# Optimization experiments

Hardware: AMD Instinct MI355X
Metric: run time of the kernel (lower is better)

Reference implementation:

```python
import jax, jax.numpy as jnp
import numpy as np

B, T, M, DK, DV, S = 64, 256, 64, 128, 256, 128
NSK, NQ = 200, 2000


def _glorot(k, shape):
    lim = np.sqrt(6.0 / (shape[0] + shape[1])).astype(np.float32)
    return jax.random.uniform(k, shape, jnp.float32, -lim, lim)


def setup_inputs() -> dict:
    key = jax.random.key(0)
    ks = jax.random.split(key, 16)
    tn = lambda k, shape: 0.1 * jax.random.truncated_normal(k, -2.0, 2.0, shape, jnp.float32)
    return {
        "q_data": jax.random.randint(ks[0], (B, T), 0, NSK + 1),
        "qa_data": jax.random.randint(ks[1], (B, T), 0, 2 * NSK + 1),
        "s_data": jax.random.randint(ks[2], (B, T), 0, NQ + 1),
        "key_memory": tn(ks[3], (M, DK)),
        "value_memory": tn(ks[4], (M, DV)),
        "Eq": 0.05 * jax.random.normal(ks[5], (NSK + 1, DK), jnp.float32),
        "Eqa": 0.05 * jax.random.normal(ks[6], (2 * NSK + 1, DV), jnp.float32),
        "Es": 0.05 * jax.random.normal(ks[7], (NQ + 1, DK), jnp.float32),
        "We": _glorot(ks[8], (DV, DV)), "be": jnp.zeros((DV,), jnp.float32),
        "Wa": _glorot(ks[9], (DV, DV)), "ba": jnp.zeros((DV,), jnp.float32),
        "Wsa": _glorot(ks[10], (DV, M)), "bsa": jnp.zeros((M,), jnp.float32),
        "Wqd1": _glorot(ks[11], (DK, S)), "bqd1": jnp.zeros((S,), jnp.float32),
        "Wqd": _glorot(ks[12], (S, 1)), "bqd": jnp.zeros((1,), jnp.float32),
        "Wsd1": _glorot(ks[13], (DK, S)), "bsd1": jnp.zeros((S,), jnp.float32),
        "Wsd": _glorot(ks[14], (S, 1)), "bsd": jnp.zeros((1,), jnp.float32),
    }


def reference(q_data, qa_data, s_data, key_memory, value_memory, Eq, Eqa, Es,
              We, be, Wa, ba, Wsa, bsa, Wqd1, bqd1, Wqd, bqd, Wsd1, bsd1, Wsd, bsd):
    b = q_data.shape[0]
    qe = Eq[q_data]    # [B,T,DK]
    qae = Eqa[qa_data]  # [B,T,DV]
    se = Es[s_data]    # [B,T,DK]
    # time-independent precomputation (same math, hoisted out of the loop)
    corr = jax.nn.softmax(jnp.einsum("btk,mk->btm", qe, key_memory), axis=-1)  # [B,T,M]
    erase = qae @ We + be  # [B,T,DV] (activation=None in source)
    add = qae @ Wa + ba    # [B,T,DV]
    qd = jnp.tanh(qe @ Wqd1 + bqd1) @ Wqd + bqd  # [B,T,1]
    sd = jnp.tanh(se @ Wsd1 + bsd1) @ Wsd + bsd  # [B,T,1]

    def step(Mv, x):
        cw, er, ad = x  # [B,M], [B,DV], [B,DV]
        read = jnp.einsum("bm,bmd->bd", cw, Mv)        # read BEFORE write
        sa1 = read @ Wsa + bsa                          # [B,M]
        sa = jnp.sum(cw * sa1, axis=1)                  # [B]
        scale = cw[:, :, None]                          # [B,M,1]
        Mv_new = Mv * (1.0 - er[:, None, :] * scale) + ad[:, None, :] * scale
        return Mv_new, sa

    Mv0 = jnp.broadcast_to(value_memory[None], (b,) + value_memory.shape)
    xs = (corr.transpose(1, 0, 2), erase.transpose(1, 0, 2), add.transpose(1, 0, 2))
    _, sa_t = jax.lax.scan(step, Mv0, xs)  # sa_t: [T,B]
    z = 3.0 * sa_t.T - qd[..., 0] - sd[..., 0]  # [B,T]
    return jax.nn.sigmoid(z)
```

## Files before the change

kernel.cpp:

```cpp
#include <hip/hip_runtime.h>
#include <math.h>

#define B_   64
#define T_   256
#define M_   64
#define DK_  128
#define DV_  256
#define S_   128
#define NQR  201
#define NQAR 401
#define NSR  2001

static __device__ __forceinline__ int imin(int a, int b){ return a < b ? a : b; }

static __device__ __forceinline__ float fast_tanh(float x){
  float e = __expf(2.f * x);
  return 1.f - 2.f / (e + 1.f);
}

template<int CTRL, int RM>
static __device__ __forceinline__ float dppadd(float x) {
  return x + __int_as_float(
      __builtin_amdgcn_update_dpp(0, __float_as_int(x), CTRL, RM, 0xf, true));
}
static __device__ __forceinline__ float wave_sum_lane63(float x) {
  x = dppadd<0x111, 0xf>(x);
  x = dppadd<0x112, 0xf>(x);
  x = dppadd<0x114, 0xf>(x);
  x = dppadd<0x118, 0xf>(x);
  x = dppadd<0x142, 0xa>(x);
  x = dppadd<0x143, 0xc>(x);
  return x;
}

__device__ void corr_role(int blk, const float* __restrict__ Eq,
                          const float* __restrict__ Km,
                          const float* __restrict__ Wsa,
                          const float* __restrict__ bsa,
                          float* __restrict__ corr,
                          float* __restrict__ w2_t,
                          float* __restrict__ csb_t)
{
  __shared__ float eq[4][DK_];
  __shared__ float cwb[4][M_];
  const int w = threadIdx.x >> 6, m = threadIdx.x & 63;
  const int i  = blk * 4 + w;
  const int ic = imin(i, NQR - 1);
  eq[w][m]      = Eq[ic * DK_ + m];
  eq[w][m + 64] = Eq[ic * DK_ + 64 + m];
  float acc = 0.f;
  const float4* kr = (const float4*)(Km + m * DK_);
  #pragma unroll 8
  for (int k4 = 0; k4 < DK_ / 4; ++k4) {
    float4 kv = kr[k4];
    acc = fmaf(eq[w][k4 * 4 + 0], kv.x, acc);
    acc = fmaf(eq[w][k4 * 4 + 1], kv.y, acc);
    acc = fmaf(eq[w][k4 * 4 + 2], kv.z, acc);
    acc = fmaf(eq[w][k4 * 4 + 3], kv.w, acc);
  }
  float mx = acc;
  #pragma unroll
  for (int off = 32; off; off >>= 1) mx = fmaxf(mx, __shfl_xor(mx, off, 64));
  float e = __expf(acc - mx);
  float ssum = e;
  #pragma unroll
  for (int off = 32; off; off >>= 1) ssum += __shfl_xor(ssum, off, 64);
  const float cw = e / ssum;
  if (i < NQR) corr[i * M_ + m] = cw;
  cwb[w][m] = cw;

  float pv = wave_sum_lane63(cw * bsa[m]);
  if (m == 63 && i < NQR) csb_t[i] = pv;

  float aw[4] = {0,0,0,0};
  for (int mm = 0; mm < M_; ++mm) {
    const float c = cwb[w][mm];
    #pragma unroll
    for (int r = 0; r < 4; ++r)
      aw[r] = fmaf(c, Wsa[(r * 64 + m) * M_ + mm], aw[r]);
  }
  if (i < NQR) {
    #pragma unroll
    for (int r = 0; r < 4; ++r) w2_t[i * DV_ + r * 64 + m] = aw[r];
  }
}

__device__ void ea_role(int blk, const float* __restrict__ Eqa,
                        const float* __restrict__ We, const float* __restrict__ be,
                        const float* __restrict__ Wa, const float* __restrict__ ba,
                        float* __restrict__ ert, float* __restrict__ adt)
{
  __shared__ float a[8][DV_];
  const int d  = threadIdx.x;
  const int i0 = blk * 8;
  #pragma unroll
  for (int r = 0; r < 8; ++r) a[r][d] = Eqa[imin(i0 + r, NQAR - 1) * DV_ + d];
  __syncthreads();
  float er[8] = {0,0,0,0,0,0,0,0}, ad[8] = {0,0,0,0,0,0,0,0};
  for (int k = 0; k < DV_; ++k) {
    float we = We[k * DV_ + d];
    float wa = Wa[k * DV_ + d];
    #pragma unroll
    for (int r = 0; r < 8; ++r) {
      er[r] = fmaf(a[r][k], we, er[r]);
      ad[r] = fmaf(a[r][k], wa, ad[r]);
    }
  }
  const float beo = be[d], bao = ba[d];
  #pragma unroll
  for (int r = 0; r < 8; ++r) {
    int i = i0 + r;
    if (i < NQAR) { ert[i * DV_ + d] = er[r] + beo; adt[i * DV_ + d] = ad[r] + bao; }
  }
}

__device__ void mlp_role(int blk, const float* __restrict__ E,
                         const float* __restrict__ W1, const float* __restrict__ b1,
                         const float* __restrict__ W2v, const float* __restrict__ b2,
                         float* __restrict__ outt, int nrows)
{
  __shared__ float e[8 * S_];
  __shared__ float red[8][2];
  const int tid = threadIdx.x;
  const int s = tid & 127, rh = tid >> 7;
  const int i0 = blk * 8;
  #pragma unroll
  for (int j = 0; j < 4; ++j) {
    int x = tid + j * 256;
    int row = imin(i0 + (x >> 7), nrows - 1);
    e[x] = E[row * DK_ + (x & 127)];
  }
  __syncthreads();
  float acc[4] = {0,0,0,0};
  const float* eb = e + rh * 4 * 128;
  for (int k = 0; k < DK_; ++k) {
    float wv = W1[k * S_ + s];
    #pragma unroll
    for (int r = 0; r < 4; ++r) acc[r] = fmaf(eb[r * 128 + k], wv, acc[r]);
  }
  const float b1s = b1[s], w2s = W2v[s];
  float p[4];
  #pragma unroll
  for (int r = 0; r < 4; ++r) p[r] = fast_tanh(acc[r] + b1s) * w2s;
  #pragma unroll
  for (int r = 0; r < 4; ++r) p[r] = wave_sum_lane63(p[r]);
  const int lane = tid & 63;
  const int half = s >> 6;
  if (lane == 63) {
    #pragma unroll
    for (int r = 0; r < 4; ++r) red[rh * 4 + r][half] = p[r];
  }
  __syncthreads();
  if (tid < 8) {
    int i = i0 + tid;
    if (i < nrows) outt[i] = red[tid][0] + red[tid][1] + b2[0];
  }
}

#define NB_CORR 51
#define NB_EA   51
#define NB_QD   26
#define NB_SD   251
#define NB_TOT  (NB_CORR + NB_EA + NB_QD + NB_SD)

__global__ __launch_bounds__(256) void tables_kernel(
    const float* Eq, const float* Km, const float* Wsa, const float* bsa,
    float* corr_t, float* w2_t, float* csb_t,
    const float* Eqa, const float* We, const float* be,
    const float* Wa, const float* ba, float* er_t, float* ad_t,
    const float* Wqd1, const float* bqd1, const float* Wqd, const float* bqd, float* qd_t,
    const float* Es, const float* Wsd1, const float* bsd1, const float* Wsd, const float* bsd, float* sd_t)
{
  int blk = blockIdx.x;
  if (blk < NB_CORR) { corr_role(blk, Eq, Km, Wsa, bsa, corr_t, w2_t, csb_t); return; }
  blk -= NB_CORR;
  if (blk < NB_EA)   { ea_role(blk, Eqa, We, be, Wa, ba, er_t, ad_t); return; }
  blk -= NB_EA;
  if (blk < NB_QD)   { mlp_role(blk, Eq, Wqd1, bqd1, Wqd, bqd, qd_t, NQR); return; }
  blk -= NB_QD;
  mlp_role(blk, Es, Wsd1, bsd1, Wsd, bsd, sd_t, NSR);
}

struct SOps { float er, ad, w2; };

static __device__ __forceinline__ void fetchg(
    int g, const int4& qq, const int4& qaq, int m0, int d,
    const float* __restrict__ corr_t, const float* __restrict__ er_t,
    const float* __restrict__ ad_t, const float* __restrict__ w2_t,
    float4 (&cA)[4], float4 (&cB)[4], SOps (&o)[4])
{
  const int q0 = __builtin_amdgcn_readlane(qq.x,  g);
  const int q1 = __builtin_amdgcn_readlane(qq.y,  g);
  const int q2 = __builtin_amdgcn_readlane(qq.z,  g);
  const int q3 = __builtin_amdgcn_readlane(qq.w,  g);
  const int a0 = __builtin_amdgcn_readlane(qaq.x, g);
  const int a1 = __builtin_amdgcn_readlane(qaq.y, g);
  const int a2 = __builtin_amdgcn_readlane(qaq.z, g);
  const int a3 = __builtin_amdgcn_readlane(qaq.w, g);
  cA[0] = *(const float4*)(corr_t + q0 * M_ + m0);
  cB[0] = *(const float4*)(corr_t + q0 * M_ + m0 + 4);
  cA[1] = *(const float4*)(corr_t + q1 * M_ + m0);
  cB[1] = *(const float4*)(corr_t + q1 * M_ + m0 + 4);
  cA[2] = *(const float4*)(corr_t + q2 * M_ + m0);
  cB[2] = *(const float4*)(corr_t + q2 * M_ + m0 + 4);
  cA[3] = *(const float4*)(corr_t + q3 * M_ + m0);
  cB[3] = *(const float4*)(corr_t + q3 * M_ + m0 + 4);
  o[0].er = er_t[a0 * DV_ + d];  o[0].ad = ad_t[a0 * DV_ + d];  o[0].w2 = w2_t[q0 * DV_ + d];
  o[1].er = er_t[a1 * DV_ + d];  o[1].ad = ad_t[a1 * DV_ + d];  o[1].w2 = w2_t[q1 * DV_ + d];
  o[2].er = er_t[a2 * DV_ + d];  o[2].ad = ad_t[a2 * DV_ + d];  o[2].w2 = w2_t[q2 * DV_ + d];
  o[3].er = er_t[a3 * DV_ + d];  o[3].ad = ad_t[a3 * DV_ + d];  o[3].w2 = w2_t[q3 * DV_ + d];
}

static __device__ __forceinline__ float stepf(
    float (&Mv)[8], const float4& ca, const float4& cb, const SOps& o)
{
  const float c[8] = {ca.x, ca.y, ca.z, ca.w, cb.x, cb.y, cb.z, cb.w};
  float r0 = c[0] * Mv[0];
  float r1 = c[1] * Mv[1];
  #pragma unroll
  for (int j = 0; j < 8; ++j) {
    if (j >= 2) {
      if (j & 1) r1 = fmaf(c[j], Mv[j], r1);
      else       r0 = fmaf(c[j], Mv[j], r0);
    }
    const float tmp = fmaf(-o.er, Mv[j], o.ad);
    Mv[j] = fmaf(c[j], tmp, Mv[j]);
  }
  return wave_sum_lane63((r0 + r1) * o.w2);
}

__global__ __launch_bounds__(512) void scan_kernel(
    const int* __restrict__ q_data, const int* __restrict__ qa_data,
    const float* __restrict__ corr_t, const float* __restrict__ er_t,
    const float* __restrict__ ad_t, const float* __restrict__ w2_t,
    const float* __restrict__ Vm, float* __restrict__ sa_part)
{
  const int b   = blockIdx.y;
  const int dq  = blockIdx.x;
  const int tid = threadIdx.x;
  const int dl  = tid & 63;
  const int w   = tid >> 6;
  const int m0  = __builtin_amdgcn_readfirstlane(w * 8);
  const int d   = dq * 64 + dl;

  const int4 qq  = ((const int4*)(q_data  + b * T_))[dl];
  const int4 qaq = ((const int4*)(qa_data + b * T_))[dl];

  float Mv[8];
  #pragma unroll
  for (int j = 0; j < 8; ++j) Mv[j] = Vm[(m0 + j) * DV_ + d];

  float* baseP = sa_part + ((dq * 8 + w) * B_ + b) * T_;

  float4 cAA[4], cBA[4], cAB[4], cBB[4];
  SOps oA[4], oB[4];
  fetchg(0, qq, qaq, m0, d, corr_t, er_t, ad_t, w2_t, cAA, cBA, oA);
  fetchg(1, qq, qaq, m0, d, corr_t, er_t, ad_t, w2_t, cAB, cBB, oB);

  for (int g = 0; g < 64; g += 2) {
    float4 pA;
    pA.x = stepf(Mv, cAA[0], cBA[0], oA[0]);
    pA.y = stepf(Mv, cAA[1], cBA[1], oA[1]);
    pA.z = stepf(Mv, cAA[2], cBA[2], oA[2]);
    pA.w = stepf(Mv, cAA[3], cBA[3], oA[3]);
    fetchg((g + 2) & 63, qq, qaq, m0, d, corr_t, er_t, ad_t, w2_t, cAA, cBA, oA);
    if (dl == 63) *(float4*)(baseP + 4 * g) = pA;

    float4 pB;
    pB.x = stepf(Mv, cAB[0], cBB[0], oB[0]);
    pB.y = stepf(Mv, cAB[1], cBB[1], oB[1]);
    pB.z = stepf(Mv, cAB[2], cBB[2], oB[2]);
    pB.w = stepf(Mv, cAB[3], cBB[3], oB[3]);
    fetchg((g + 3) & 63, qq, qaq, m0, d, corr_t, er_t, ad_t, w2_t, cAB, cBB, oB);
    if (dl == 63) *(float4*)(baseP + 4 * g + 4) = pB;
  }
}

__global__ __launch_bounds__(256) void final_kernel(
    const int* __restrict__ q_data, const int* __restrict__ s_data,
    const float* __restrict__ sa_part, const float* __restrict__ csb_t,
    const float* __restrict__ qd_t, const float* __restrict__ sd_t,
    float* __restrict__ out)
{
  const int b = blockIdx.x, t = threadIdx.x;
  float s = 0.f;
  #pragma unroll
  for (int p = 0; p < 32; ++p) s += sa_part[(p * B_ + b) * T_ + t];
  const int bt = b * T_ + t;
  const int q  = q_data[bt];
  const int si = s_data[bt];
  const float sa = s + csb_t[q];
  const float z = 3.f * sa - qd_t[q] - sd_t[si];
  out[bt] = 1.f / (1.f + __expf(-z));
}

extern "C" void kernel_launch(void* const* d_in, const int* in_sizes, int n_in,
                              void* d_out, int out_size, void* d_ws, size_t ws_size,
                              hipStream_t stream)
{
  const int*   q_data = (const int*)d_in[0];
  const int*   qa_data= (const int*)d_in[1];
  const int*   s_data = (const int*)d_in[2];
  const float* Km     = (const float*)d_in[3];
  const float* Vm     = (const float*)d_in[4];
  const float* Eq     = (const float*)d_in[5];
  const float* Eqa    = (const float*)d_in[6];
  const float* Es     = (const float*)d_in[7];
  const float* We     = (const float*)d_in[8];
  const float* be     = (const float*)d_in[9];
  const float* Wa     = (const float*)d_in[10];
  const float* ba     = (const float*)d_in[11];
  const float* Wsa    = (const float*)d_in[12];
  const float* bsa    = (const float*)d_in[13];
  const float* Wqd1   = (const float*)d_in[14];
  const float* bqd1   = (const float*)d_in[15];
  const float* Wqd    = (const float*)d_in[16];
  const float* bqd    = (const float*)d_in[17];
  const float* Wsd1   = (const float*)d_in[18];
  const float* bsd1   = (const float*)d_in[19];
  const float* Wsd    = (const float*)d_in[20];
  const float* bsd    = (const float*)d_in[21];
  float* out = (float*)d_out;

  float* wsf    = (float*)d_ws;
  float* corr_t = wsf;
  float* w2_t   = corr_t + NQR * M_;
  float* csb_t  = w2_t + NQR * DV_;
  float* er_t   = csb_t + 204;
  float* ad_t   = er_t + NQAR * DV_;
  float* qd_t   = ad_t + NQAR * DV_;
  float* sd_t   = qd_t + 204;
  float* sa_p   = sd_t + 2004;

  tables_kernel<<<NB_TOT, 256, 0, stream>>>(
      Eq, Km, Wsa, bsa, corr_t, w2_t, csb_t,
      Eqa, We, be, Wa, ba, er_t, ad_t,
      Wqd1, bqd1, Wqd, bqd, qd_t,
      Es, Wsd1, bsd1, Wsd, bsd, sd_t);
  scan_kernel<<<dim3(4, B_), 512, 0, stream>>>(q_data, qa_data, corr_t, er_t, ad_t, w2_t, Vm, sa_p);
  final_kernel<<<B_, 256, 0, stream>>>(q_data, s_data, sa_p, csb_t, qd_t, sd_t, out);
}
```

Baseline: 173.6 us.

## Give each scan wave sixteen memory rows and reduce within sixteen-lane rows

The scan kernel now runs 256 threads per block instead of 512. Each wave owns 16 memory slots instead of 8, and dot-product partials are reduced only across 16-lane DPP rows, which drops the cross-row broadcast steps. That doubles the number of partial sums the final kernel must add, and the sa_part workspace grows to match. Separately, the Wsa contraction in the table-building pass now reads weights as float4. The intent is fewer reduction instructions per step, at the cost of fewer resident waves and more register state per thread.

```diff
diff --git a/kernel.cpp b/kernel.cpp
--- a/kernel.cpp
+++ b/kernel.cpp
@@ -30,6 +30,13 @@
   x = dppadd<0x118, 0xf>(x);
   x = dppadd<0x142, 0xa>(x);
   x = dppadd<0x143, 0xc>(x);
+  return x;
+}
+static __device__ __forceinline__ float row_sum_lane15(float x) {
+  x = dppadd<0x111, 0xf>(x);
+  x = dppadd<0x112, 0xf>(x);
+  x = dppadd<0x114, 0xf>(x);
+  x = dppadd<0x118, 0xf>(x);
   return x;
 }
 
@@ -73,11 +80,15 @@
   if (m == 63 && i < NQR) csb_t[i] = pv;
 
   float aw[4] = {0,0,0,0};
-  for (int mm = 0; mm < M_; ++mm) {
-    const float c = cwb[w][mm];
-    #pragma unroll
-    for (int r = 0; r < 4; ++r)
-      aw[r] = fmaf(c, Wsa[(r * 64 + m) * M_ + mm], aw[r]);
+  for (int mm4 = 0; mm4 < M_ / 4; ++mm4) {
+    #pragma unroll
+    for (int r = 0; r < 4; ++r) {
+      float4 wv = *(const float4*)(Wsa + (r * 64 + m) * M_ + mm4 * 4);
+      aw[r] = fmaf(cwb[w][mm4 * 4 + 0], wv.x, aw[r]);
+      aw[r] = fmaf(cwb[w][mm4 * 4 + 1], wv.y, aw[r]);
+      aw[r] = fmaf(cwb[w][mm4 * 4 + 2], wv.z, aw[r]);
+      aw[r] = fmaf(cwb[w][mm4 * 4 + 3], wv.w, aw[r]);
+    }
   }
   if (i < NQR) {
     #pragma unroll
@@ -181,55 +192,62 @@
   mlp_role(blk, Es, Wsd1, bsd1, Wsd, bsd, sd_t, NSR);
 }
 
-struct SOps { float er, ad, w2; };
-
-static __device__ __forceinline__ void fetchg(
-    int g, const int4& qq, const int4& qaq, int m0, int d,
+struct TOps { float er, ad, w2; };
+
+template<bool HI>
+static __device__ __forceinline__ void fetch2(
+    int l, const int4& qq, const int4& qaq, int m0, int d,
     const float* __restrict__ corr_t, const float* __restrict__ er_t,
     const float* __restrict__ ad_t, const float* __restrict__ w2_t,
-    float4 (&cA)[4], float4 (&cB)[4], SOps (&o)[4])
-{
-  const int q0 = __builtin_amdgcn_readlane(qq.x,  g);
-  const int q1 = __builtin_amdgcn_readlane(qq.y,  g);
-  const int q2 = __builtin_amdgcn_readlane(qq.z,  g);
-  const int q3 = __builtin_amdgcn_readlane(qq.w,  g);
-  const int a0 = __builtin_amdgcn_readlane(qaq.x, g);
-  const int a1 = __builtin_amdgcn_readlane(qaq.y, g);
-  const int a2 = __builtin_amdgcn_readlane(qaq.z, g);
-  const int a3 = __builtin_amdgcn_readlane(qaq.w, g);
-  cA[0] = *(const float4*)(corr_t + q0 * M_ + m0);
-  cB[0] = *(const float4*)(corr_t + q0 * M_ + m0 + 4);
-  cA[1] = *(const float4*)(corr_t + q1 * M_ + m0);
-  cB[1] = *(const float4*)(corr_t + q1 * M_ + m0 + 4);
-  cA[2] = *(const float4*)(corr_t + q2 * M_ + m0);
-  cB[2] = *(const float4*)(corr_t + q2 * M_ + m0 + 4);
-  cA[3] = *(const float4*)(corr_t + q3 * M_ + m0);
-  cB[3] = *(const float4*)(corr_t + q3 * M_ + m0 + 4);
-  o[0].er = er_t[a0 * DV_ + d];  o[0].ad = ad_t[a0 * DV_ + d];  o[0].w2 = w2_t[q0 * DV_ + d];
-  o[1].er = er_t[a1 * DV_ + d];  o[1].ad = ad_t[a1 * DV_ + d];  o[1].w2 = w2_t[q1 * DV_ + d];
-  o[2].er = er_t[a2 * DV_ + d];  o[2].ad = ad_t[a2 * DV_ + d];  o[2].w2 = w2_t[q2 * DV_ + d];
-  o[3].er = er_t[a3 * DV_ + d];  o[3].ad = ad_t[a3 * DV_ + d];  o[3].w2 = w2_t[q3 * DV_ + d];
+    float4 (&c)[2][4], TOps (&o)[2])
+{
+  const int q0 = __builtin_amdgcn_readlane(HI ? qq.z  : qq.x,  l);
+  const int q1 = __builtin_amdgcn_readlane(HI ? qq.w  : qq.y,  l);
+  const int a0 = __builtin_amdgcn_readlane(HI ? qaq.z : qaq.x, l);
+  const int a1 = __builtin_amdgcn_readlane(HI ? qaq.w : qaq.y, l);
+  const float* cp0 = corr_t + q0 * M_ + m0;
+  const float* cp1 = corr_t + q1 * M_ + m0;
+  c[0][0] = *(const float4*)(cp0);
+  c[0][1] = *(const float4*)(cp0 + 4);
+  c[0][2] = *(const float4*)(cp0 + 8);
+  c[0][3] = *(const float4*)(cp0 + 12);
+  c[1][0] = *(const float4*)(cp1);
+  c[1][1] = *(const float4*)(cp1 + 4);
+  c[1][2] = *(const float4*)(cp1 + 8);
+  c[1][3] = *(const float4*)(cp1 + 12);
+  const float* e0 = er_t + a0 * DV_;
+  const float* e1 = er_t + a1 * DV_;
+  const float* ad0 = ad_t + a0 * DV_;
+  const float* ad1 = ad_t + a1 * DV_;
+  const float* w0 = w2_t + q0 * DV_;
+  const float* w1 = w2_t + q1 * DV_;
+  o[0].er = e0[d];  o[0].ad = ad0[d];  o[0].w2 = w0[d];
+  o[1].er = e1[d];  o[1].ad = ad1[d];  o[1].w2 = w1[d];
 }
 
 static __device__ __forceinline__ float stepf(
-    float (&Mv)[8], const float4& ca, const float4& cb, const SOps& o)
-{
-  const float c[8] = {ca.x, ca.y, ca.z, ca.w, cb.x, cb.y, cb.z, cb.w};
-  float r0 = c[0] * Mv[0];
-  float r1 = c[1] * Mv[1];
-  #pragma unroll
-  for (int j = 0; j < 8; ++j) {
-    if (j >= 2) {
-      if (j & 1) r1 = fmaf(c[j], Mv[j], r1);
-      else       r0 = fmaf(c[j], Mv[j], r0);
+    float (&Mv)[16], const float4 (&c)[4], const TOps& o)
+{
+  float r0 = c[0].x * Mv[0];
+  float r1 = c[0].y * Mv[1];
+  #pragma unroll
+  for (int k = 0; k < 4; ++k) {
+    const float cx = c[k].x, cy = c[k].y, cz = c[k].z, cw = c[k].w;
+    if (k > 0) {
+      r0 = fmaf(cx, Mv[4 * k + 0], r0);
+      r1 = fmaf(cy, Mv[4 * k + 1], r1);
     }
-    const float tmp = fmaf(-o.er, Mv[j], o.ad);
-    Mv[j] = fmaf(c[j], tmp, Mv[j]);
-  }
-  return wave_sum_lane63((r0 + r1) * o.w2);
-}
-
-__global__ __launch_bounds__(512) void scan_kernel(
+    Mv[4 * k + 0] = fmaf(cx, fmaf(-o.er, Mv[4 * k + 0], o.ad), Mv[4 * k + 0]);
+    Mv[4 * k + 1] = fmaf(cy, fmaf(-o.er, Mv[4 * k + 1], o.ad), Mv[4 * k + 1]);
+    r0 = fmaf(cz, Mv[4 * k + 2], r0);
+    r1 = fmaf(cw, Mv[4 * k + 3], r1);
+    Mv[4 * k + 2] = fmaf(cz, fmaf(-o.er, Mv[4 * k + 2], o.ad), Mv[4 * k + 2]);
+    Mv[4 * k + 3] = fmaf(cw, fmaf(-o.er, Mv[4 * k + 3], o.ad), Mv[4 * k + 3]);
+  }
+  return row_sum_lane15((r0 + r1) * o.w2);
+}
+
+__global__ __launch_bounds__(256) void scan_kernel(
     const int* __restrict__ q_data, const int* __restrict__ qa_data,
     const float* __restrict__ corr_t, const float* __restrict__ er_t,
     const float* __restrict__ ad_t, const float* __restrict__ w2_t,
@@ -239,40 +257,34 @@
   const int dq  = blockIdx.x;
   const int tid = threadIdx.x;
   const int dl  = tid & 63;
-  const int w   = tid >> 6;
-  const int m0  = __builtin_amdgcn_readfirstlane(w * 8);
+  const int mg  = tid >> 6;
+  const int m0  = __builtin_amdgcn_readfirstlane(mg * 16);
   const int d   = dq * 64 + dl;
+  const int sub = dl >> 4;
 
   const int4 qq  = ((const int4*)(q_data  + b * T_))[dl];
   const int4 qaq = ((const int4*)(qa_data + b * T_))[dl];
 
-  float Mv[8];
-  #pragma unroll
-  for (int j = 0; j < 8; ++j) Mv[j] = Vm[(m0 + j) * DV_ + d];
-
-  float* baseP = sa_part + ((dq * 8 + w) * B_ + b) * T_;
-
-  float4 cAA[4], cBA[4], cAB[4], cBB[4];
-  SOps oA[4], oB[4];
-  fetchg(0, qq, qaq, m0, d, corr_t, er_t, ad_t, w2_t, cAA, cBA, oA);
-  fetchg(1, qq, qaq, m0, d, corr_t, er_t, ad_t, w2_t, cAB, cBB, oB);
-
-  for (int g = 0; g < 64; g += 2) {
-    float4 pA;
-    pA.x = stepf(Mv, cAA[0], cBA[0], oA[0]);
-    pA.y = stepf(Mv, cAA[1], cBA[1], oA[1]);
-    pA.z = stepf(Mv, cAA[2], cBA[2], oA[2]);
-    pA.w = stepf(Mv, cAA[3], cBA[3], oA[3]);
-    fetchg((g + 2) & 63, qq, qaq, m0, d, corr_t, er_t, ad_t, w2_t, cAA, cBA, oA);
-    if (dl == 63) *(float4*)(baseP + 4 * g) = pA;
-
-    float4 pB;
-    pB.x = stepf(Mv, cAB[0], cBB[0], oB[0]);
-    pB.y = stepf(Mv, cAB[1], cBB[1], oB[1]);
-    pB.z = stepf(Mv, cAB[2], cBB[2], oB[2]);
-    pB.w = stepf(Mv, cAB[3], cBB[3], oB[3]);
-    fetchg((g + 3) & 63, qq, qaq, m0, d, corr_t, er_t, ad_t, w2_t, cAB, cBB, oB);
-    if (dl == 63) *(float4*)(baseP + 4 * g + 4) = pB;
+  float Mv[16];
+  #pragma unroll
+  for (int j = 0; j < 16; ++j) Mv[j] = Vm[(m0 + j) * DV_ + d];
+
+  float* baseP = sa_part + ((dq * 16 + mg * 4 + sub) * B_ + b) * T_;
+
+  float4 cA[2][4], cB[2][4];
+  TOps oA[2], oB[2];
+  fetch2<false>(0, qq, qaq, m0, d, corr_t, er_t, ad_t, w2_t, cA, oA);
+  fetch2<true >(0, qq, qaq, m0, d, corr_t, er_t, ad_t, w2_t, cB, oB);
+
+  for (int i = 0; i < 64; ++i) {
+    float4 p;
+    p.x = stepf(Mv, cA[0], oA[0]);
+    p.y = stepf(Mv, cA[1], oA[1]);
+    fetch2<false>((i + 1) & 63, qq, qaq, m0, d, corr_t, er_t, ad_t, w2_t, cA, oA);
+    p.z = stepf(Mv, cB[0], oB[0]);
+    p.w = stepf(Mv, cB[1], oB[1]);
+    fetch2<true >((i + 1) & 63, qq, qaq, m0, d, corr_t, er_t, ad_t, w2_t, cB, oB);
+    if ((dl & 15) == 15) *(float4*)(baseP + 4 * i) = p;
   }
 }
 
@@ -285,7 +297,7 @@
   const int b = blockIdx.x, t = threadIdx.x;
   float s = 0.f;
   #pragma unroll
-  for (int p = 0; p < 32; ++p) s += sa_part[(p * B_ + b) * T_ + t];
+  for (int p = 0; p < 64; ++p) s += sa_part[(p * B_ + b) * T_ + t];
   const int bt = b * T_ + t;
   const int q  = q_data[bt];
   const int si = s_data[bt];
@@ -337,6 +349,6 @@
       Eqa, We, be, Wa, ba, er_t, ad_t,
       Wqd1, bqd1, Wqd, bqd, qd_t,
       Es, Wsd1, bsd1, Wsd, bsd, sd_t);
-  scan_kernel<<<dim3(4, B_), 512, 0, stream>>>(q_data, qa_data, corr_t, er_t, ad_t, w2_t, Vm, sa_p);
+  scan_kernel<<<dim3(4, B_), 256, 0, stream>>>(q_data, qa_data, corr_t, er_t, ad_t, w2_t, Vm, sa_p);
   final_kernel<<<B_, 256, 0, stream>>>(q_data, s_data, sa_p, csb_t, qd_t, sd_t, out);
 }
```

Result: slower. 178.5 us (+2.8%).
